# Optimization experiments

Hardware: AMD Instinct MI355X
Metric: run time of the kernel (lower is better)

The kernel has to match this reference:

```python
import jax, jax.numpy as jnp
import numpy as np

N_NODES = 50000
N_EDGES = 1600000
IN_FEATS = 128
HIDDEN = 16
HEADS = 8
SLOPE = 0.2


def setup_inputs() -> dict:
    key = jax.random.key(0)
    ks = jax.random.split(key, 9)
    feat = jax.random.normal(ks[0], (N_NODES, IN_FEATS), dtype=jnp.float32)
    edge_src = jax.random.randint(ks[1], (N_EDGES,), 0, N_NODES, dtype=jnp.int32)
    edge_dst = jax.random.randint(ks[2], (N_EDGES,), 0, N_NODES, dtype=jnp.int32)
    # layer 0: in=128 -> H*F=128 ; layer 1: in=128 (concat of layer 0) -> 128
    s0 = 1.0 / np.sqrt(IN_FEATS)
    W0 = jax.random.normal(ks[3], (IN_FEATS, HEADS * HIDDEN), dtype=jnp.float32) * s0
    al0 = jax.random.normal(ks[4], (HEADS, HIDDEN), dtype=jnp.float32) * 0.1
    ar0 = jax.random.normal(ks[5], (HEADS, HIDDEN), dtype=jnp.float32) * 0.1
    W1 = jax.random.normal(ks[6], (HEADS * HIDDEN, HEADS * HIDDEN), dtype=jnp.float32) * s0
    al1 = jax.random.normal(ks[7], (HEADS, HIDDEN), dtype=jnp.float32) * 0.1
    ar1 = jax.random.normal(ks[8], (HEADS, HIDDEN), dtype=jnp.float32) * 0.1
    return {"feat": feat, "edge_src": edge_src, "edge_dst": edge_dst,
            "W0": W0, "al0": al0, "ar0": ar0, "W1": W1, "al1": al1, "ar1": ar1}


def _gat_conv(feat, W, al, ar, src, dst):
    """One DGL-style GATConv: no bias, no residual, no dropout, no activation."""
    n = feat.shape[0]
    h = (feat @ W).reshape(n, HEADS, HIDDEN)              # [N,H,F]
    el = jnp.sum(h * al, axis=-1)                          # [N,H]
    er = jnp.sum(h * ar, axis=-1)                          # [N,H]
    e = jax.nn.leaky_relu(el[src] + er[dst], negative_slope=SLOPE)  # [E,H]
    # edge softmax over incoming edges of each dst node
    m = jax.ops.segment_max(e, dst, num_segments=n)        # [N,H]
    ex = jnp.exp(e - m[dst])                               # [E,H]
    denom = jax.ops.segment_sum(ex, dst, num_segments=n)   # [N,H]
    alpha = ex / jnp.where(denom[dst] > 0, denom[dst], 1.0)
    # message passing: gather src features, weight, scatter-add to dst
    out = jax.ops.segment_sum(h[src] * alpha[:, :, None], dst, num_segments=n)
    return out                                             # [N,H,F]


def reference(feat, edge_src, edge_dst, W0, al0, ar0, W1, al1, ar1):
    n = feat.shape[0]
    # step 1 + concat (flatten heads)
    x = _gat_conv(feat, W0, al0, ar0, edge_src, edge_dst).reshape(n, HEADS * HIDDEN)
    # step 2 + concat
    x = _gat_conv(x, W1, al1, ar1, edge_src, edge_dst).reshape(n, HEADS * HIDDEN)
    return x
```

## Files before the change

kernel.cpp:

```cpp
#include <hip/hip_runtime.h>
#include <hip/hip_bf16.h>


#define HEADS 8
#define HID 16
#define HF 128
#define SLOPE 0.2f

#define BSHIFT 8
#define BRANGE 256
#define CHUNK 4096

typedef __attribute__((ext_vector_type(8))) short bf16x8;
typedef __attribute__((ext_vector_type(4))) float f32x4;

static __device__ __forceinline__ unsigned int f2bf(float f) {
    unsigned int u = __float_as_uint(f);
    u += 0x7fffu + ((u >> 16) & 1u);
    return u >> 16;
}


__global__ __launch_bounds__(512) void bucket_hist_kernel(
    const int* __restrict__ dst, int* __restrict__ bcount, int E, int nb) {
    __shared__ int h[BRANGE];
    int t = threadIdx.x;
    if (t < BRANGE) h[t] = 0;
    __syncthreads();
    int base = blockIdx.x * CHUNK;
    int end = base + CHUNK; if (end > E) end = E;
    for (int i = base + t; i < end; i += 512)
        atomicAdd(&h[dst[i] >> BSHIFT], 1);
    __syncthreads();
    if (t < nb && h[t]) atomicAdd(&bcount[t], h[t]);
}

__global__ __launch_bounds__(256) void bucket_scan_kernel(
    const int* __restrict__ bcount, int* __restrict__ bbase,
    int* __restrict__ gcur, int* __restrict__ rowptr, int nb, int N, int E) {
    __shared__ int s[256];
    int t = threadIdx.x;
    s[t] = (t < nb) ? bcount[t] : 0;
    __syncthreads();
    #pragma unroll
    for (int off = 1; off < 256; off <<= 1) {
        int v = (t >= off) ? s[t - off] : 0;
        __syncthreads();
        s[t] += v;
        __syncthreads();
    }
    int excl = (t == 0) ? 0 : s[t - 1];
    if (t < nb) { bbase[t] = excl; gcur[t] = excl; }
    if (t == 0) { bbase[nb] = E; rowptr[N] = E; }
}

__global__ __launch_bounds__(512) void bucket_scatter_kernel(
    const int* __restrict__ src, const int* __restrict__ dst,
    int* __restrict__ gcur, int* __restrict__ stage, int E, int nb) {
    __shared__ int hist[BRANGE];
    __shared__ int lscan[BRANGE];
    __shared__ int lcur[BRANGE];
    __shared__ int boff[BRANGE];
    __shared__ int sstage[CHUNK];
    int t = threadIdx.x;
    if (t < BRANGE) hist[t] = 0;
    __syncthreads();
    int base = blockIdx.x * CHUNK;
    int end = base + CHUNK; if (end > E) end = E;

    for (int i = base + t; i < end; i += 512)
        atomicAdd(&hist[dst[i] >> BSHIFT], 1);
    __syncthreads();

    if (t < 256) lscan[t] = hist[t];
    __syncthreads();
    #pragma unroll
    for (int off = 1; off < 256; off <<= 1) {
        int v = 0;
        if (t < 256 && t >= off) v = lscan[t - off];
        __syncthreads();
        if (t < 256) lscan[t] += v;
        __syncthreads();
    }
    int ex = 0;
    if (t < 256) ex = (t == 0) ? 0 : lscan[t - 1];
    __syncthreads();
    if (t < 256) {
        lcur[t] = ex;
        lscan[t] = ex;
        if (t < nb && hist[t] > 0) boff[t] = atomicAdd(&gcur[t], hist[t]);
    }
    __syncthreads();

    for (int i = base + t; i < end; i += 512) {
        int d = dst[i];
        int b = d >> BSHIFT;
        int pos = atomicAdd(&lcur[b], 1);
        sstage[pos] = (src[i] & 0xFFFF) | ((d & (BRANGE - 1)) << 16) | (b << 24);
    }
    __syncthreads();

    int total = end - base;
    for (int i = t; i < total; i += 512) {
        int p = sstage[i];
        int b = ((unsigned)p) >> 24;
        int gpos = boff[b] + (i - lscan[b]);
        stage[gpos] = p;
    }
}

__global__ __launch_bounds__(512) void bucket_csr_kernel(
    const int* __restrict__ stage, const int* __restrict__ bbase,
    int* __restrict__ rowptr, int* __restrict__ col, int N, int nb) {
    __shared__ int hist[BRANGE];
    __shared__ int lscan[BRANGE];
    __shared__ int lcur[BRANGE];
    int b = blockIdx.x;
    int t = threadIdx.x;
    int e0 = bbase[b], e1 = bbase[b + 1];
    if (t < BRANGE) hist[t] = 0;
    __syncthreads();
    for (int i = e0 + t; i < e1; i += 512)
        atomicAdd(&hist[(stage[i] >> 16) & (BRANGE - 1)], 1);
    __syncthreads();
    if (t < 256) lscan[t] = hist[t];
    __syncthreads();
    #pragma unroll
    for (int off = 1; off < 256; off <<= 1) {
        int v = 0;
        if (t < 256 && t >= off) v = lscan[t - off];
        __syncthreads();
        if (t < 256) lscan[t] += v;
        __syncthreads();
    }
    if (t < 256) {
        int ex = (t == 0) ? 0 : lscan[t - 1];
        lcur[t] = ex;
        int node = (b << BSHIFT) + t;
        if (node < N) rowptr[node] = e0 + ex;
    }
    __syncthreads();
    for (int i = e0 + t; i < e1; i += 512) {
        int p = stage[i];
        int pos = e0 + atomicAdd(&lcur[(p >> 16) & (BRANGE - 1)], 1);
        col[pos] = p & 0xFFFF;
    }
}


__global__ __launch_bounds__(256) void wtrans_kernel(const float* __restrict__ W,
                                                     unsigned short* __restrict__ Wtb) {
    int gid = blockIdx.x * 256 + threadIdx.x;
    int c = gid >> 3;
    int k0 = (gid & 7) * 16;
    #pragma unroll
    for (int q = 0; q < 4; ++q) {
        int k = k0 + q * 4;
        ushort4 o = make_ushort4(
            (unsigned short)f2bf(W[(k + 0) * HF + c]),
            (unsigned short)f2bf(W[(k + 1) * HF + c]),
            (unsigned short)f2bf(W[(k + 2) * HF + c]),
            (unsigned short)f2bf(W[(k + 3) * HF + c]));
        *(ushort4*)(Wtb + (size_t)c * HF + k) = o;
    }
}


__global__ __launch_bounds__(256) void gemm_mfma_kernel(
    const float* __restrict__ X, const unsigned short* __restrict__ Wtb,
    const float* __restrict__ AL, const float* __restrict__ AR,
    unsigned short* __restrict__ Hb, float* __restrict__ EL,
    float* __restrict__ ER, int n) {
    __shared__ __align__(16) unsigned short xs[64 * HF];
    __shared__ __align__(16) unsigned short ws[HF * HF];
    int t = threadIdx.x;
    int row0 = blockIdx.x * 64;

    {
        int r = t >> 2;
        int k0 = (t & 3) * 32;
        int gr = row0 + r;
        float4 f[8];
        if (gr < n) {
            const float4* p = (const float4*)(X + (size_t)gr * HF + k0);
            #pragma unroll
            for (int i = 0; i < 8; ++i) f[i] = p[i];
        } else {
            #pragma unroll
            for (int i = 0; i < 8; ++i) f[i] = make_float4(0.f, 0.f, 0.f, 0.f);
        }
        unsigned int rowbase = r * 256;
        unsigned int sw = (r & 7) << 4;
        #pragma unroll
        for (int g2 = 0; g2 < 4; ++g2) {
            float4 a = f[g2 * 2], b = f[g2 * 2 + 1];
            int4 pk;
            pk.x = (int)(f2bf(a.x) | (f2bf(a.y) << 16));
            pk.y = (int)(f2bf(a.z) | (f2bf(a.w) << 16));
            pk.z = (int)(f2bf(b.x) | (f2bf(b.y) << 16));
            pk.w = (int)(f2bf(b.z) | (f2bf(b.w) << 16));
            unsigned int addr = rowbase + ((unsigned)((k0 + g2 * 8) * 2) ^ sw);
            *(int4*)((char*)xs + addr) = pk;
        }
    }
    {
        int c = t >> 1;
        unsigned int kb0 = (t & 1) * 128;
        const int4* src = (const int4*)((const char*)Wtb + (size_t)c * 256 + kb0);
        unsigned int sw = (c & 7) << 4;
        #pragma unroll
        for (int i = 0; i < 8; ++i) {
            int4 v = src[i];
            unsigned int addr = c * 256 + ((kb0 + i * 16) ^ sw);
            *(int4*)((char*)ws + addr) = v;
        }
    }
    __syncthreads();

    int wv = t >> 6;
    int l = t & 63;
    int lr = l & 15;
    int g = l >> 4;

    bf16x8 bfr[4];
    {
        int r = wv * 16 + lr;
        unsigned int rowbase = r * 256;
        unsigned int sw = (r & 7) << 4;
        #pragma unroll
        for (int s = 0; s < 4; ++s) {
            unsigned int kbyte = (unsigned)((s * 32 + g * 8) * 2);
            bfr[s] = *(bf16x8*)((char*)xs + rowbase + (kbyte ^ sw));
        }
    }

    f32x4 acc[8];
    #pragma unroll
    for (int ct = 0; ct < 8; ++ct) acc[ct] = (f32x4){0.f, 0.f, 0.f, 0.f};

    #pragma unroll
    for (int ct = 0; ct < 8; ++ct) {
        int c = ct * 16 + lr;
        unsigned int rowbase = c * 256;
        unsigned int sw = (c & 7) << 4;
        #pragma unroll
        for (int s = 0; s < 4; ++s) {
            unsigned int kbyte = (unsigned)((s * 32 + g * 8) * 2);
            bf16x8 af = *(bf16x8*)((char*)ws + rowbase + (kbyte ^ sw));
            acc[ct] = __builtin_amdgcn_mfma_f32_16x16x32_bf16(af, bfr[s], acc[ct], 0, 0, 0);
        }
    }

    int grow = row0 + wv * 16 + lr;
    bool valid = grow < n;

    if (valid) {
        #pragma unroll
        for (int ct = 0; ct < 8; ++ct) {
            ushort4 hb4 = make_ushort4(
                (unsigned short)f2bf(acc[ct][0]), (unsigned short)f2bf(acc[ct][1]),
                (unsigned short)f2bf(acc[ct][2]), (unsigned short)f2bf(acc[ct][3]));
            *(ushort4*)(Hb + (size_t)grow * HF + ct * 16 + g * 4) = hb4;
        }
    }

    #pragma unroll
    for (int ct = 0; ct < 8; ++ct) {
        float e1 = 0.f, e2 = 0.f;
        #pragma unroll
        for (int rg = 0; rg < 4; ++rg) {
            float alv = AL[ct * 16 + g * 4 + rg];
            float arv = AR[ct * 16 + g * 4 + rg];
            e1 += acc[ct][rg] * alv;
            e2 += acc[ct][rg] * arv;
        }
        e1 += __shfl_xor(e1, 16); e1 += __shfl_xor(e1, 32);
        e2 += __shfl_xor(e2, 16); e2 += __shfl_xor(e2, 32);
        if (g == 0 && valid) {
            EL[grow * HEADS + ct] = e1;
            ER[grow * HEADS + ct] = e2;
        }
    }
}


__global__ __launch_bounds__(256) void gat_aggregate_kernel(
    const unsigned int* __restrict__ HbU,
    const float* __restrict__ EL, const float* __restrict__ ER,
    const int* __restrict__ rowptr, const int* __restrict__ col,
    float* __restrict__ OUT, int n) {
    int wid = (int)((blockIdx.x * blockDim.x + threadIdx.x) >> 6);
    if (wid >= n) return;
    int lane = threadIdx.x & 63;
    int s0 = rowptr[wid], s1 = rowptr[wid + 1];
    size_t ob = (size_t)wid * HF;
    if (s1 == s0) {
        ((float2*)(OUT + ob))[lane] = make_float2(0.f, 0.f);
        return;
    }

    int h = lane & 7;
    int j = lane >> 3;
    int hC = lane >> 3;
    float er_h = ER[wid * HEADS + h];

    float accx = 0.f, accy = 0.f;
    float dpart = 0.f;

    for (int base = s0; base < s1; base += 8) {
        int i = base + j;
        int icl = i < s1 ? i : s1 - 1;
        int sj = col[icl];
        float e = EL[sj * HEADS + h] + er_h;
        e = fmaxf(e, SLOPE * e);
        float w = __expf(e);
        if (i >= s1) w = 0.f;
        dpart += w;

        if (base + 8 <= s1) {
            #pragma unroll
            for (int jj = 0; jj < 8; ++jj) {
                float wC = __shfl(w, jj * 8 + hC);
                int s = __builtin_amdgcn_readlane(sj, jj * 8);
                unsigned int pv = HbU[(size_t)s * 64 + lane];
                accx += wC * __uint_as_float(pv << 16);
                accy += wC * __uint_as_float(pv & 0xffff0000u);
            }
        } else {
            int ne = s1 - base;
            for (int jj = 0; jj < ne; ++jj) {
                float wC = __shfl(w, jj * 8 + hC);
                int s = __builtin_amdgcn_readlane(sj, jj * 8);
                unsigned int pv = HbU[(size_t)s * 64 + lane];
                accx += wC * __uint_as_float(pv << 16);
                accy += wC * __uint_as_float(pv & 0xffff0000u);
            }
        }
    }

    dpart += __shfl_xor(dpart, 8);
    dpart += __shfl_xor(dpart, 16);
    dpart += __shfl_xor(dpart, 32);
    float rC = 1.f / __shfl(dpart, hC);

    ((float2*)(OUT + ob))[lane] = make_float2(accx * rC, accy * rC);
}


extern "C" void kernel_launch(void* const* d_in, const int* in_sizes, int n_in,
                              void* d_out, int out_size, void* d_ws, size_t ws_size,
                              hipStream_t stream) {
    const float* feat = (const float*)d_in[0];
    const int*   esrc = (const int*)d_in[1];
    const int*   edst = (const int*)d_in[2];
    const float* W0   = (const float*)d_in[3];
    const float* al0  = (const float*)d_in[4];
    const float* ar0  = (const float*)d_in[5];
    const float* W1   = (const float*)d_in[6];
    const float* al1  = (const float*)d_in[7];
    const float* ar1  = (const float*)d_in[8];
    float* out = (float*)d_out;

    const int N = in_sizes[0] / HF;
    const int E = in_sizes[1];
    const int nb = (N + BRANGE - 1) >> BSHIFT;

    char* w = (char*)d_ws;
    auto alloc = [&](size_t bytes) -> void* {
        void* p = (void*)w;
        w += (bytes + 255) & ~(size_t)255;
        return p;
    };
    unsigned short* hb   = (unsigned short*)alloc((size_t)N * HF * 2);
    float* x1     = (float*)alloc((size_t)N * HF * 4);
    float* el_buf = (float*)alloc((size_t)N * HEADS * 4);
    float* er_buf = (float*)alloc((size_t)N * HEADS * 4);
    int*   rowptr = (int*)alloc((size_t)(N + 1) * 4);
    int*   col    = (int*)alloc((size_t)E * 4);
    int*   bcount = (int*)alloc((size_t)nb * 4);
    int*   bbase  = (int*)alloc((size_t)(nb + 1) * 4);
    int*   gcur   = (int*)alloc((size_t)nb * 4);
    unsigned short* wtb0 = (unsigned short*)alloc((size_t)HF * HF * 2);
    unsigned short* wtb1 = (unsigned short*)alloc((size_t)HF * HF * 2);
    int*   stage  = (int*)x1;

    wtrans_kernel<<<4, 256, 0, stream>>>(W0, wtb0);
    wtrans_kernel<<<4, 256, 0, stream>>>(W1, wtb1);

    hipMemsetAsync(bcount, 0, (size_t)nb * 4, stream);
    int gChunk = (E + CHUNK - 1) / CHUNK;
    bucket_hist_kernel<<<gChunk, 512, 0, stream>>>(edst, bcount, E, nb);
    bucket_scan_kernel<<<1, 256, 0, stream>>>(bcount, bbase, gcur, rowptr, nb, N, E);
    bucket_scatter_kernel<<<gChunk, 512, 0, stream>>>(esrc, edst, gcur, stage, E, nb);
    bucket_csr_kernel<<<nb, 512, 0, stream>>>(stage, bbase, rowptr, col, N, nb);

    int gGemm = (N + 63) / 64;
    int gAgg  = (N * 64 + 255) / 256;

    gemm_mfma_kernel<<<gGemm, 256, 0, stream>>>(feat, wtb0, al0, ar0, hb, el_buf, er_buf, N);
    gat_aggregate_kernel<<<gAgg, 256, 0, stream>>>((const unsigned int*)hb, el_buf, er_buf,
                                                   rowptr, col, x1, N);

    gemm_mfma_kernel<<<gGemm, 256, 0, stream>>>(x1, wtb1, al1, ar1, hb, el_buf, er_buf, N);
    gat_aggregate_kernel<<<gAgg, 256, 0, stream>>>((const unsigned int*)hb, el_buf, er_buf,
                                                   rowptr, col, out, N);
}
```

Before: 233.5 us.

## Split GAT aggregation into four head-pair passes over a 2D grid

```diff
diff --git a/kernel.cpp b/kernel.cpp
--- a/kernel.cpp
+++ b/kernel.cpp
@@ -284,66 +284,61 @@
 }
 
 
-__global__ __launch_bounds__(256) void gat_aggregate_kernel(
+__global__ __launch_bounds__(256) void gat_aggregate_pass_kernel(
     const unsigned int* __restrict__ HbU,
     const float* __restrict__ EL, const float* __restrict__ ER,
     const int* __restrict__ rowptr, const int* __restrict__ col,
     float* __restrict__ OUT, int n) {
     int wid = (int)((blockIdx.x * blockDim.x + threadIdx.x) >> 6);
     if (wid >= n) return;
+    int pass = blockIdx.y;
     int lane = threadIdx.x & 63;
     int s0 = rowptr[wid], s1 = rowptr[wid + 1];
-    size_t ob = (size_t)wid * HF;
-    if (s1 == s0) {
-        ((float2*)(OUT + ob))[lane] = make_float2(0.f, 0.f);
-        return;
-    }
-
-    int h = lane & 7;
-    int j = lane >> 3;
-    int hC = lane >> 3;
-    float er_h = ER[wid * HEADS + h];
-
-    float accx = 0.f, accy = 0.f;
-    float dpart = 0.f;
-
-    for (int base = s0; base < s1; base += 8) {
+
+    int j = lane >> 1;
+    int hh = lane & 1;
+    int ph0 = pass * 2;
+    float er_h = ER[wid * HEADS + ph0 + hh];
+    int cpair = lane & 15;
+    int hsel = cpair >> 3;
+
+    float accx = 0.f, accy = 0.f, dpart = 0.f;
+
+    for (int base = s0; base < s1; base += 32) {
         int i = base + j;
         int icl = i < s1 ? i : s1 - 1;
-        int sj = col[icl];
-        float e = EL[sj * HEADS + h] + er_h;
+        int sj = __builtin_nontemporal_load(&col[icl]);
+        float e = EL[sj * HEADS + ph0 + hh] + er_h;
         e = fmaxf(e, SLOPE * e);
         float w = __expf(e);
         if (i >= s1) w = 0.f;
         dpart += w;
 
-        if (base + 8 <= s1) {
-            #pragma unroll
-            for (int jj = 0; jj < 8; ++jj) {
-                float wC = __shfl(w, jj * 8 + hC);
-                int s = __builtin_amdgcn_readlane(sj, jj * 8);
-                unsigned int pv = HbU[(size_t)s * 64 + lane];
-                accx += wC * __uint_as_float(pv << 16);
-                accy += wC * __uint_as_float(pv & 0xffff0000u);
-            }
-        } else {
-            int ne = s1 - base;
-            for (int jj = 0; jj < ne; ++jj) {
-                float wC = __shfl(w, jj * 8 + hC);
-                int s = __builtin_amdgcn_readlane(sj, jj * 8);
-                unsigned int pv = HbU[(size_t)s * 64 + lane];
-                accx += wC * __uint_as_float(pv << 16);
-                accy += wC * __uint_as_float(pv & 0xffff0000u);
-            }
-        }
-    }
-
-    dpart += __shfl_xor(dpart, 8);
-    dpart += __shfl_xor(dpart, 16);
+        int ng = s1 - base; if (ng > 32) ng = 32;
+        int nit = (ng + 3) >> 2;
+        for (int it = 0; it < nit; ++it) {
+            int e4 = it * 4 + (lane >> 4);
+            float wC = __shfl(w, e4 * 2 + hsel);
+            int s = __shfl(sj, e4 * 2);
+            unsigned int pv = HbU[(size_t)s * 64 + pass * 16 + cpair];
+            accx += wC * __uint_as_float(pv << 16);
+            accy += wC * __uint_as_float(pv & 0xffff0000u);
+        }
+    }
+
+    accx += __shfl_xor(accx, 16); accx += __shfl_xor(accx, 32);
+    accy += __shfl_xor(accy, 16); accy += __shfl_xor(accy, 32);
+    dpart += __shfl_xor(dpart, 2);  dpart += __shfl_xor(dpart, 4);
+    dpart += __shfl_xor(dpart, 8);  dpart += __shfl_xor(dpart, 16);
     dpart += __shfl_xor(dpart, 32);
-    float rC = 1.f / __shfl(dpart, hC);
-
-    ((float2*)(OUT + ob))[lane] = make_float2(accx * rC, accy * rC);
+
+    if (lane < 16) {
+        float d = __shfl(dpart, hsel);
+        float rC = (s1 > s0) ? 1.f / d : 0.f;
+        float* op = OUT + (size_t)wid * HF + pass * 32 + cpair * 2;
+        __builtin_nontemporal_store(accx * rC, op);
+        __builtin_nontemporal_store(accy * rC, op + 1);
+    }
 }
 
 
@@ -395,13 +390,13 @@
     bucket_csr_kernel<<<nb, 512, 0, stream>>>(stage, bbase, rowptr, col, N, nb);
 
     int gGemm = (N + 63) / 64;
-    int gAgg  = (N * 64 + 255) / 256;
+    dim3 gAgg((N * 64 + 255) / 256, 4);
 
     gemm_mfma_kernel<<<gGemm, 256, 0, stream>>>(feat, wtb0, al0, ar0, hb, el_buf, er_buf, N);
-    gat_aggregate_kernel<<<gAgg, 256, 0, stream>>>((const unsigned int*)hb, el_buf, er_buf,
-                                                   rowptr, col, x1, N);
+    gat_aggregate_pass_kernel<<<gAgg, 256, 0, stream>>>((const unsigned int*)hb, el_buf,
+                                                        er_buf, rowptr, col, x1, N);
 
     gemm_mfma_kernel<<<gGemm, 256, 0, stream>>>(x1, wtb1, al1, ar1, hb, el_buf, er_buf, N);
-    gat_aggregate_kernel<<<gAgg, 256, 0, stream>>>((const unsigned int*)hb, el_buf, er_buf,
-                                                   rowptr, col, out, N);
-}
+    gat_aggregate_pass_kernel<<<gAgg, 256, 0, stream>>>((const unsigned int*)hb, el_buf,
+                                                        er_buf, rowptr, col, out, N);
+}
```

New measurement: 430.3 us. 84.3% more time.
